# Performance work log

Hardware: AMD Instinct MI355X
Metric: run time of the kernel (lower is better)

## Reference

```python
import jax, jax.numpy as jnp
import numpy as np

N = 50000   # nodes
E = 1600000 # edges
D = 128     # input_dim
H = 128     # hidden_dim
O = 128     # output_dim
G = 64      # graphs in batch
EPS = 1e-5  # batchnorm eps


def setup_inputs() -> dict:
    key = jax.random.key(0)
    ks = jax.random.split(key, 20)
    x = jax.random.normal(ks[0], (N, D), jnp.float32)
    edge_index = jax.random.randint(ks[1], (2, E), 0, N, dtype=jnp.int32)
    batch = jnp.sort(jax.random.randint(ks[2], (N,), 0, G, dtype=jnp.int32))

    def lin(k, fi, fo):
        return jax.random.normal(k, (fi, fo), jnp.float32) / np.float32(np.sqrt(fi))

    return {
        "x": x, "edge_index": edge_index, "batch": batch,
        "W1": lin(ks[3], D, H), "b1": jnp.zeros((H,), jnp.float32),
        "W2": lin(ks[4], H, H), "b2": jnp.zeros((H,), jnp.float32),
        "W3": lin(ks[5], H, O), "b3": jnp.zeros((O,), jnp.float32),
        "g1": 1.0 + 0.1 * jax.random.normal(ks[6], (H,), jnp.float32),
        "be1": 0.1 * jax.random.normal(ks[7], (H,), jnp.float32),
        "rm1": 0.1 * jax.random.normal(ks[8], (H,), jnp.float32),
        "rv1": 0.5 + jax.random.uniform(ks[9], (H,), jnp.float32),
        "g2": 1.0 + 0.1 * jax.random.normal(ks[10], (H,), jnp.float32),
        "be2": 0.1 * jax.random.normal(ks[11], (H,), jnp.float32),
        "rm2": 0.1 * jax.random.normal(ks[12], (H,), jnp.float32),
        "rv2": 0.5 + jax.random.uniform(ks[13], (H,), jnp.float32),
    }


def _gcn_layer(h, W, b, row, col, norm):
    # h: [N, Fin] -> [N, Fout]; GCN: A_hat @ (h W) + b with sym-normalized A_hat
    h = h @ W
    msg = h[row] * norm[:, None]                      # [E+N, Fout] gather
    out = jax.ops.segment_sum(msg, col, num_segments=N)
    return out + b


def _bn_eval(h, g, be, rm, rv):
    return (h - rm) * jax.lax.rsqrt(rv + EPS) * g + be


def reference(x, edge_index, batch, W1, b1, W2, b2, W3, b3,
              g1, be1, rm1, rv1, g2, be2, rm2, rv2):
    # add self loops (PyG GCNConv default)
    loop = jnp.arange(N, dtype=edge_index.dtype)
    row = jnp.concatenate([edge_index[0], loop])
    col = jnp.concatenate([edge_index[1], loop])
    deg = jax.ops.segment_sum(jnp.ones_like(col, jnp.float32), col, num_segments=N)
    dinv = jnp.where(deg > 0, jax.lax.rsqrt(jnp.maximum(deg, 1.0)), 0.0)
    norm = dinv[row] * dinv[col]                       # [E+N]

    h = _gcn_layer(x, W1, b1, row, col, norm)
    h = jax.nn.relu(_bn_eval(h, g1, be1, rm1, rv1))    # dropout is identity (eval)
    h = _gcn_layer(h, W2, b2, row, col, norm)
    h = jax.nn.relu(_bn_eval(h, g2, be2, rm2, rv2))
    h = _gcn_layer(h, W3, b3, row, col, norm)
    # global_add_pool by graph id
    return jax.ops.segment_sum(h, batch, num_segments=G)  # [G, O]
```

## Files before the change

### kernel.cpp

```cpp
#include <hip/hip_runtime.h>
#include <hip/hip_bf16.h>

#define NN 50000
#define NROWS (NN + 1)
#define NE 1600000
#define NEPAD 1951024
#define DIM 128
#define NG 64
#define EPSV 1e-5f
#define NCHUNK 49
#define UNROLL 8
#define RUN 4
#define NXCD 8
#define SHARD_COLS (NN / NXCD)
#define FILL_CHUNKS 256

typedef __attribute__((ext_vector_type(8))) __bf16 bf16x8;
typedef __attribute__((ext_vector_type(2))) __bf16 bf16x2;
typedef __attribute__((ext_vector_type(16))) float f32x16;


__global__ void count_kernel(const int4* __restrict__ ecol4, int* __restrict__ cnt) {
    int i = blockIdx.x * 256 + threadIdx.x;
    if (i < NE / 4) {
        int4 c = ecol4[i];
        atomicAdd(&cnt[c.x], 1);
        atomicAdd(&cnt[c.y], 1);
        atomicAdd(&cnt[c.z], 1);
        atomicAdd(&cnt[c.w], 1);
    }
}

__global__ void scan_chunk(const int* __restrict__ cnt, int* __restrict__ excl,
                           int* __restrict__ csum) {
    __shared__ int lds[256];
    int t = threadIdx.x;
    int base = blockIdx.x * 1024 + t * 4;
    int v0 = (base + 0 < NN) ? ((cnt[base + 0] + 7) & ~7) : 0;
    int v1 = (base + 1 < NN) ? ((cnt[base + 1] + 7) & ~7) : 0;
    int v2 = (base + 2 < NN) ? ((cnt[base + 2] + 7) & ~7) : 0;
    int v3 = (base + 3 < NN) ? ((cnt[base + 3] + 7) & ~7) : 0;
    int s = v0 + v1 + v2 + v3;
    lds[t] = s;
    __syncthreads();
    for (int off = 1; off < 256; off <<= 1) {
        int x = (t >= off) ? lds[t - off] : 0;
        __syncthreads();
        lds[t] += x;
        __syncthreads();
    }
    int run = lds[t] - s;
    if (t == 255) csum[blockIdx.x] = lds[t];
    if (base + 0 < NN) excl[base + 0] = run; run += v0;
    if (base + 1 < NN) excl[base + 1] = run; run += v1;
    if (base + 2 < NN) excl[base + 2] = run; run += v2;
    if (base + 3 < NN) excl[base + 3] = run;
}

__global__ void scan_tail(const int* __restrict__ csum, int* __restrict__ coff,
                          int* __restrict__ row_ptr, int nch) {
    int l = threadIdx.x;
    int v = (l < nch) ? csum[l] : 0;
    int s = v;
    for (int o = 1; o < 64; o <<= 1) {
        int x = __shfl_up(s, o);
        if (l >= o) s += x;
    }
    if (l < nch) coff[l] = s - v;
    if (l == nch - 1) row_ptr[NN] = s;
}

__global__ void fixup_kernel(int* __restrict__ row_ptr, const int* __restrict__ coff,
                             const int* __restrict__ cnt, float* __restrict__ dinv,
                             int* __restrict__ cursor) {
    int n = blockIdx.x * 256 + threadIdx.x;
    if (n < NN) {
        int rp = row_ptr[n] + coff[n >> 10];
        row_ptr[n] = rp;
        cursor[n] = rp;
        dinv[n] = rsqrtf((float)(cnt[n] + 1));
    }
}

__global__ void sentinel_kernel(int4* __restrict__ esrc4) {
    const int4 v = {NN, NN, NN, NN};
    for (int i = blockIdx.x * 256 + threadIdx.x; i < NEPAD / 4; i += gridDim.x * 256)
        esrc4[i] = v;
}

__global__ void fill_kernel(const int* __restrict__ erow, const int* __restrict__ ecol,
                            int* __restrict__ cursor, int* __restrict__ esrc) {
    const int shard = blockIdx.x & (NXCD - 1);
    const int chunk = blockIdx.x >> 3;
    const int lo = shard * SHARD_COLS;
    const int hi = lo + SHARD_COLS;
    for (int e = chunk * 256 + threadIdx.x; e < NE; e += FILL_CHUNKS * 256) {
        const int c = ecol[e];
        if (c >= lo && c < hi) {
            int pos = atomicAdd(&cursor[c], 1);
            esrc[pos] = erow[e];
        }
    }
}

__global__ void bn_prep_kernel(const float* __restrict__ b1, const float* __restrict__ g1,
                               const float* __restrict__ be1, const float* __restrict__ rm1,
                               const float* __restrict__ rv1,
                               const float* __restrict__ b2, const float* __restrict__ g2,
                               const float* __restrict__ be2, const float* __restrict__ rm2,
                               const float* __restrict__ rv2,
                               float* __restrict__ sc1, float* __restrict__ sh1,
                               float* __restrict__ sc2, float* __restrict__ sh2,
                               __bf16* __restrict__ tbuf) {
    int c = threadIdx.x;
    if (c < DIM) {
        float s1 = g1[c] * rsqrtf(rv1[c] + EPSV);
        sc1[c] = s1;
        sh1[c] = (b1[c] - rm1[c]) * s1 + be1[c];
        float s2 = g2[c] * rsqrtf(rv2[c] + EPSV);
        sc2[c] = s2;
        sh2[c] = (b2[c] - rm2[c]) * s2 + be2[c];
        tbuf[(size_t)NN * DIM + c] = (__bf16)0.f;
    }
}


__device__ __forceinline__ bf16x8 load8(const float* p) {
    float4 lo = ((const float4*)p)[0], hi = ((const float4*)p)[1];
    bf16x8 a;
    a[0] = (__bf16)lo.x; a[1] = (__bf16)lo.y; a[2] = (__bf16)lo.z; a[3] = (__bf16)lo.w;
    a[4] = (__bf16)hi.x; a[5] = (__bf16)hi.y; a[6] = (__bf16)hi.z; a[7] = (__bf16)hi.w;
    return a;
}
__device__ __forceinline__ bf16x8 load8(const __bf16* p) {
    return *(const bf16x8*)p;
}

template <typename T>
__global__ void __launch_bounds__(256) matmul_kernel(const T* __restrict__ h,
                                                     const float* __restrict__ W,
                                                     const float* __restrict__ dinv,
                                                     __bf16* __restrict__ t) {
    const int wave = threadIdx.x >> 6;
    const int lane = threadIdx.x & 63;
    const int col = wave * 32 + (lane & 31);
    const int khalf = (lane >> 5) * 8;

    bf16x8 b[8];
#pragma unroll
    for (int kc = 0; kc < 8; kc++) {
#pragma unroll
        for (int j = 0; j < 8; j++) {
            b[kc][j] = (__bf16)W[(kc * 16 + khalf + j) * DIM + col];
        }
    }

    const int ntiles = (NN + 31) / 32;
    for (int tile = blockIdx.x; tile < ntiles; tile += gridDim.x) {
        const int arow = tile * 32 + (lane & 31);
        const int arow_c = (arow < NN) ? arow : (NN - 1);
        f32x16 acc = {};
#pragma unroll
        for (int kc = 0; kc < 8; kc++) {
            bf16x8 a = load8(h + (size_t)arow_c * DIM + kc * 16 + khalf);
            acc = __builtin_amdgcn_mfma_f32_32x32x16_bf16(a, b[kc], acc, 0, 0, 0);
        }
#pragma unroll
        for (int r = 0; r < 16; r++) {
            int orow = tile * 32 + (r & 3) + 8 * (r >> 2) + 4 * (lane >> 5);
            if (orow < NN) t[(size_t)orow * DIM + col] = (__bf16)(acc[r] * dinv[orow]);
        }
    }
}


__device__ __forceinline__ float lo16(unsigned u) { return __uint_as_float(u << 16); }
__device__ __forceinline__ float hi16(unsigned u) { return __uint_as_float(u & 0xffff0000u); }

__device__ __forceinline__ void gather_core(
    const unsigned* __restrict__ t32, const int* __restrict__ esrc,
    int beg, int end, int lane, float& ax, float& ay) {
    for (int e = beg; e < end; e += UNROLL) {
        int s[UNROLL];
        unsigned u[UNROLL];
#pragma unroll
        for (int i = 0; i < UNROLL; i++) s[i] = esrc[e + i];
#pragma unroll
        for (int i = 0; i < UNROLL; i++) {
            const unsigned idx = ((unsigned)s[i] << 6) + lane;
            u[i] = t32[idx];
        }
#pragma unroll
        for (int i = 0; i < UNROLL; i++) {
            ax += lo16(u[i]);
            ay += hi16(u[i]);
        }
    }
}

__global__ void __launch_bounds__(256) gather_bn_kernel(
    const unsigned* __restrict__ t32, const int* __restrict__ row_ptr,
    const int* __restrict__ esrc, const float* __restrict__ dinv,
    const float* __restrict__ scale, const float* __restrict__ shift,
    __bf16* __restrict__ out) {
    const int lane = threadIdx.x & 63;
    const int n = __builtin_amdgcn_readfirstlane(blockIdx.x * 4 + (threadIdx.x >> 6));
    if (n >= NN) return;
    float ax = 0.f, ay = 0.f;
    const int beg = row_ptr[n], end = row_ptr[n + 1];
    gather_core(t32, esrc, beg, end, lane, ax, ay);
    {
        const unsigned u = t32[((unsigned)n << 6) + lane];
        ax += lo16(u); ay += hi16(u);
    }
    const float dv = dinv[n];
    const int c0 = lane * 2, c1 = c0 + 1;
    const float vx = fmaxf(fmaf(ax, dv * scale[c0], shift[c0]), 0.f);
    const float vy = fmaxf(fmaf(ay, dv * scale[c1], shift[c1]), 0.f);
    bf16x2 o; o[0] = (__bf16)vx; o[1] = (__bf16)vy;
    *(bf16x2*)(out + (size_t)n * DIM + c0) = o;
}


__global__ void __launch_bounds__(256) gather_pool_kernel(
    const unsigned* __restrict__ t32, const int* __restrict__ row_ptr,
    const int* __restrict__ esrc, const float* __restrict__ dinv,
    const float* __restrict__ bias, const int* __restrict__ batch,
    float* __restrict__ out) {
    const int lane = threadIdx.x & 63;
    const int wid = __builtin_amdgcn_readfirstlane(blockIdx.x * 4 + (threadIdx.x >> 6));
    const int n0 = wid * RUN;
    if (n0 >= NN) return;
    const int c0 = lane * 2, c1 = c0 + 1;
    const float bx = bias[c0], by = bias[c1];
    float rx = 0.f, ry = 0.f;
    int g = batch[n0];
    for (int j = 0; j < RUN; j++) {
        const int n = n0 + j;
        float ax = 0.f, ay = 0.f;
        const int beg = row_ptr[n], end = row_ptr[n + 1];
        gather_core(t32, esrc, beg, end, lane, ax, ay);
        {
            const unsigned u = t32[((unsigned)n << 6) + lane];
            ax += lo16(u); ay += hi16(u);
        }
        const float dv = dinv[n];
        const int gn = batch[n];
        if (gn != g) {
            atomicAdd(out + (size_t)g * DIM + c0, rx);
            atomicAdd(out + (size_t)g * DIM + c1, ry);
            rx = 0.f; ry = 0.f; g = gn;
        }
        rx += fmaf(ax, dv, bx);
        ry += fmaf(ay, dv, by);
    }
    atomicAdd(out + (size_t)g * DIM + c0, rx);
    atomicAdd(out + (size_t)g * DIM + c1, ry);
}


extern "C" void kernel_launch(void* const* d_in, const int* in_sizes, int n_in,
                              void* d_out, int out_size, void* d_ws, size_t ws_size,
                              hipStream_t stream) {
    const float* x    = (const float*)d_in[0];
    const int*   ei   = (const int*)d_in[1];
    const int*   batch= (const int*)d_in[2];
    const float* W1 = (const float*)d_in[3];
    const float* b1 = (const float*)d_in[4];
    const float* W2 = (const float*)d_in[5];
    const float* b2 = (const float*)d_in[6];
    const float* W3 = (const float*)d_in[7];
    const float* b3 = (const float*)d_in[8];
    const float* g1 = (const float*)d_in[9];
    const float* be1= (const float*)d_in[10];
    const float* rm1= (const float*)d_in[11];
    const float* rv1= (const float*)d_in[12];
    const float* g2 = (const float*)d_in[13];
    const float* be2= (const float*)d_in[14];
    const float* rm2= (const float*)d_in[15];
    const float* rv2= (const float*)d_in[16];
    const int* erow = ei;
    const int* ecol = ei + NE;

    char* ws = (char*)d_ws;
    size_t off = 0;
    auto alloc = [&](size_t bytes) -> void* {
        void* p = ws + off;
        off = (off + bytes + 255) & ~(size_t)255;
        return p;
    };
    int*    cnt     = (int*)alloc(NN * sizeof(int));
    int*    row_ptr = (int*)alloc((NN + 1) * sizeof(int));
    int*    cursor  = (int*)alloc(NN * sizeof(int));
    int*    csum    = (int*)alloc(64 * sizeof(int));
    int*    coff    = (int*)alloc(64 * sizeof(int));
    float*  dinv    = (float*)alloc(NN * sizeof(float));
    int*    esrc    = (int*)alloc(NEPAD * sizeof(int));
    __bf16* tbuf    = (__bf16*)alloc((size_t)NROWS * DIM * sizeof(__bf16));
    __bf16* hbuf    = (__bf16*)alloc((size_t)NN * DIM * sizeof(__bf16));
    float*  sc1     = (float*)alloc(DIM * sizeof(float));
    float*  sh1     = (float*)alloc(DIM * sizeof(float));
    float*  sc2     = (float*)alloc(DIM * sizeof(float));
    float*  sh2     = (float*)alloc(DIM * sizeof(float));

    hipMemsetAsync(cnt, 0, NN * sizeof(int), stream);
    hipMemsetAsync(d_out, 0, NG * DIM * sizeof(float), stream);

    bn_prep_kernel<<<1, 128, 0, stream>>>(b1, g1, be1, rm1, rv1,
                                          b2, g2, be2, rm2, rv2,
                                          sc1, sh1, sc2, sh2, tbuf);
    sentinel_kernel<<<1024, 256, 0, stream>>>((int4*)esrc);
    count_kernel<<<(NE / 4 + 255) / 256, 256, 0, stream>>>((const int4*)ecol, cnt);
    scan_chunk<<<NCHUNK, 256, 0, stream>>>(cnt, row_ptr, csum);
    scan_tail<<<1, 64, 0, stream>>>(csum, coff, row_ptr, NCHUNK);
    fixup_kernel<<<(NN + 255) / 256, 256, 0, stream>>>(row_ptr, coff, cnt, dinv, cursor);
    fill_kernel<<<NXCD * FILL_CHUNKS, 256, 0, stream>>>(erow, ecol, cursor, esrc);

    const unsigned* t32 = (const unsigned*)tbuf;
    const int nblk = (NN + 3) / 4;
    const int nblk_pool = (NN / RUN + 3) / 4;

    matmul_kernel<float><<<512, 256, 0, stream>>>(x, W1, dinv, tbuf);
    gather_bn_kernel<<<nblk, 256, 0, stream>>>(t32, row_ptr, esrc, dinv,
                                               sc1, sh1, hbuf);
    matmul_kernel<__bf16><<<512, 256, 0, stream>>>(hbuf, W2, dinv, tbuf);
    gather_bn_kernel<<<nblk, 256, 0, stream>>>(t32, row_ptr, esrc, dinv,
                                               sc2, sh2, hbuf);
    matmul_kernel<__bf16><<<512, 256, 0, stream>>>(hbuf, W3, dinv, tbuf);
    gather_pool_kernel<<<nblk_pool, 256, 0, stream>>>(t32, row_ptr, esrc, dinv,
                                                      b3, batch, (float*)d_out);
}
```

Measured before the change: 385.5 us.

## Gather neighbor rows with 16-byte loads across four edge groups per wave

The gather kernels now split each wave into four 16-lane groups. Each lane loads a uint4 (8 bf16 features), so one wave fetches 4 neighbor rows per load instead of one row via 32-bit loads. Partial sums are reduced with xor shuffles, and only 16 lanes finish the BN/ReLU or pooling and write vectorized outputs. The aim is fewer, wider memory transactions per edge and more gather parallelism, at the cost of extra shuffles and idle lanes in the epilogue. Separately, the sentinel fill is fused into the count kernel to save a launch.

```diff
diff --git a/kernel.cpp b/kernel.cpp
--- a/kernel.cpp
+++ b/kernel.cpp
@@ -9,25 +9,34 @@
 #define NG 64
 #define EPSV 1e-5f
 #define NCHUNK 49
-#define UNROLL 8
 #define RUN 4
 #define NXCD 8
 #define SHARD_COLS (NN / NXCD)
 #define FILL_CHUNKS 256
+#define SENT_BLOCKS 512
 
 typedef __attribute__((ext_vector_type(8))) __bf16 bf16x8;
 typedef __attribute__((ext_vector_type(2))) __bf16 bf16x2;
 typedef __attribute__((ext_vector_type(16))) float f32x16;
 
 
-__global__ void count_kernel(const int4* __restrict__ ecol4, int* __restrict__ cnt) {
-    int i = blockIdx.x * 256 + threadIdx.x;
-    if (i < NE / 4) {
-        int4 c = ecol4[i];
-        atomicAdd(&cnt[c.x], 1);
-        atomicAdd(&cnt[c.y], 1);
-        atomicAdd(&cnt[c.z], 1);
-        atomicAdd(&cnt[c.w], 1);
+__global__ void count_sent_kernel(const int4* __restrict__ ecol4,
+                                  int* __restrict__ cnt,
+                                  int4* __restrict__ esrc4) {
+    if (blockIdx.x < SENT_BLOCKS) {
+        const int4 v = {NN, NN, NN, NN};
+        for (int i = blockIdx.x * 256 + threadIdx.x; i < NEPAD / 4;
+             i += SENT_BLOCKS * 256)
+            esrc4[i] = v;
+    } else {
+        int i = (blockIdx.x - SENT_BLOCKS) * 256 + threadIdx.x;
+        if (i < NE / 4) {
+            int4 c = ecol4[i];
+            atomicAdd(&cnt[c.x], 1);
+            atomicAdd(&cnt[c.y], 1);
+            atomicAdd(&cnt[c.z], 1);
+            atomicAdd(&cnt[c.w], 1);
+        }
     }
 }
 
@@ -80,12 +89,6 @@
         cursor[n] = rp;
         dinv[n] = rsqrtf((float)(cnt[n] + 1));
     }
-}
-
-__global__ void sentinel_kernel(int4* __restrict__ esrc4) {
-    const int4 v = {NN, NN, NN, NN};
-    for (int i = blockIdx.x * 256 + threadIdx.x; i < NEPAD / 4; i += gridDim.x * 256)
-        esrc4[i] = v;
 }
 
 __global__ void fill_kernel(const int* __restrict__ erow, const int* __restrict__ ecol,
@@ -177,85 +180,116 @@
 __device__ __forceinline__ float lo16(unsigned u) { return __uint_as_float(u << 16); }
 __device__ __forceinline__ float hi16(unsigned u) { return __uint_as_float(u & 0xffff0000u); }
 
-__device__ __forceinline__ void gather_core(
-    const unsigned* __restrict__ t32, const int* __restrict__ esrc,
-    int beg, int end, int lane, float& ax, float& ay) {
-    for (int e = beg; e < end; e += UNROLL) {
-        int s[UNROLL];
-        unsigned u[UNROLL];
-#pragma unroll
-        for (int i = 0; i < UNROLL; i++) s[i] = esrc[e + i];
-#pragma unroll
-        for (int i = 0; i < UNROLL; i++) {
-            const unsigned idx = ((unsigned)s[i] << 6) + lane;
-            u[i] = t32[idx];
-        }
-#pragma unroll
-        for (int i = 0; i < UNROLL; i++) {
-            ax += lo16(u[i]);
-            ay += hi16(u[i]);
-        }
+__device__ __forceinline__ void accum8(uint4 u, float (&a)[8]) {
+    a[0] += lo16(u.x); a[1] += hi16(u.x);
+    a[2] += lo16(u.y); a[3] += hi16(u.y);
+    a[4] += lo16(u.z); a[5] += hi16(u.z);
+    a[6] += lo16(u.w); a[7] += hi16(u.w);
+}
+
+__device__ __forceinline__ void gather_core4(
+    const uint4* __restrict__ tp4, const int* __restrict__ esrc,
+    int beg, int end, int grp, int sub, float (&a)[8]) {
+    for (int e = beg; e < end; e += 8) {
+        const int s0 = esrc[e + grp];
+        const int s1 = esrc[e + 4 + grp];
+        const uint4 u0 = tp4[(unsigned)s0 * 16u + sub];
+        const uint4 u1 = tp4[(unsigned)s1 * 16u + sub];
+        accum8(u0, a);
+        accum8(u1, a);
     }
 }
 
 __global__ void __launch_bounds__(256) gather_bn_kernel(
-    const unsigned* __restrict__ t32, const int* __restrict__ row_ptr,
+    const uint4* __restrict__ tp4, const int* __restrict__ row_ptr,
     const int* __restrict__ esrc, const float* __restrict__ dinv,
     const float* __restrict__ scale, const float* __restrict__ shift,
     __bf16* __restrict__ out) {
     const int lane = threadIdx.x & 63;
+    const int grp = lane >> 4, sub = lane & 15;
     const int n = __builtin_amdgcn_readfirstlane(blockIdx.x * 4 + (threadIdx.x >> 6));
     if (n >= NN) return;
-    float ax = 0.f, ay = 0.f;
+    float a[8] = {};
     const int beg = row_ptr[n], end = row_ptr[n + 1];
-    gather_core(t32, esrc, beg, end, lane, ax, ay);
-    {
-        const unsigned u = t32[((unsigned)n << 6) + lane];
-        ax += lo16(u); ay += hi16(u);
-    }
-    const float dv = dinv[n];
-    const int c0 = lane * 2, c1 = c0 + 1;
-    const float vx = fmaxf(fmaf(ax, dv * scale[c0], shift[c0]), 0.f);
-    const float vy = fmaxf(fmaf(ay, dv * scale[c1], shift[c1]), 0.f);
-    bf16x2 o; o[0] = (__bf16)vx; o[1] = (__bf16)vy;
-    *(bf16x2*)(out + (size_t)n * DIM + c0) = o;
+    gather_core4(tp4, esrc, beg, end, grp, sub, a);
+#pragma unroll
+    for (int i = 0; i < 8; i++) {
+        a[i] += __shfl_xor(a[i], 16);
+        a[i] += __shfl_xor(a[i], 32);
+    }
+    if (lane < 16) {
+        accum8(tp4[(unsigned)n * 16u + sub], a);
+        const float dv = dinv[n];
+        const int c0 = sub * 8;
+        float4 s0 = *(const float4*)(scale + c0), s1 = *(const float4*)(scale + c0 + 4);
+        float4 h0 = *(const float4*)(shift + c0), h1 = *(const float4*)(shift + c0 + 4);
+        bf16x8 o;
+        o[0] = (__bf16)fmaxf(fmaf(a[0], dv * s0.x, h0.x), 0.f);
+        o[1] = (__bf16)fmaxf(fmaf(a[1], dv * s0.y, h0.y), 0.f);
+        o[2] = (__bf16)fmaxf(fmaf(a[2], dv * s0.z, h0.z), 0.f);
+        o[3] = (__bf16)fmaxf(fmaf(a[3], dv * s0.w, h0.w), 0.f);
+        o[4] = (__bf16)fmaxf(fmaf(a[4], dv * s1.x, h1.x), 0.f);
+        o[5] = (__bf16)fmaxf(fmaf(a[5], dv * s1.y, h1.y), 0.f);
+        o[6] = (__bf16)fmaxf(fmaf(a[6], dv * s1.z, h1.z), 0.f);
+        o[7] = (__bf16)fmaxf(fmaf(a[7], dv * s1.w, h1.w), 0.f);
+        *(bf16x8*)(out + (size_t)n * DIM + c0) = o;
+    }
 }
 
 
 __global__ void __launch_bounds__(256) gather_pool_kernel(
-    const unsigned* __restrict__ t32, const int* __restrict__ row_ptr,
+    const uint4* __restrict__ tp4, const int* __restrict__ row_ptr,
     const int* __restrict__ esrc, const float* __restrict__ dinv,
     const float* __restrict__ bias, const int* __restrict__ batch,
     float* __restrict__ out) {
     const int lane = threadIdx.x & 63;
+    const int grp = lane >> 4, sub = lane & 15;
     const int wid = __builtin_amdgcn_readfirstlane(blockIdx.x * 4 + (threadIdx.x >> 6));
     const int n0 = wid * RUN;
     if (n0 >= NN) return;
-    const int c0 = lane * 2, c1 = c0 + 1;
-    const float bx = bias[c0], by = bias[c1];
-    float rx = 0.f, ry = 0.f;
+    const int c0 = sub * 8;
+    float4 b0 = *(const float4*)(bias + c0), b1v = *(const float4*)(bias + c0 + 4);
+    float rx[8] = {};
     int g = batch[n0];
     for (int j = 0; j < RUN; j++) {
         const int n = n0 + j;
-        float ax = 0.f, ay = 0.f;
+        float a[8] = {};
         const int beg = row_ptr[n], end = row_ptr[n + 1];
-        gather_core(t32, esrc, beg, end, lane, ax, ay);
-        {
-            const unsigned u = t32[((unsigned)n << 6) + lane];
-            ax += lo16(u); ay += hi16(u);
+        gather_core4(tp4, esrc, beg, end, grp, sub, a);
+#pragma unroll
+        for (int i = 0; i < 8; i++) {
+            a[i] += __shfl_xor(a[i], 16);
+            a[i] += __shfl_xor(a[i], 32);
         }
         const float dv = dinv[n];
         const int gn = batch[n];
         if (gn != g) {
-            atomicAdd(out + (size_t)g * DIM + c0, rx);
-            atomicAdd(out + (size_t)g * DIM + c1, ry);
-            rx = 0.f; ry = 0.f; g = gn;
-        }
-        rx += fmaf(ax, dv, bx);
-        ry += fmaf(ay, dv, by);
-    }
-    atomicAdd(out + (size_t)g * DIM + c0, rx);
-    atomicAdd(out + (size_t)g * DIM + c1, ry);
+            if (lane < 16) {
+                float* op = out + (size_t)g * DIM + c0;
+#pragma unroll
+                for (int i = 0; i < 8; i++) atomicAdd(op + i, rx[i]);
+            }
+#pragma unroll
+            for (int i = 0; i < 8; i++) rx[i] = 0.f;
+            g = gn;
+        }
+        if (lane < 16) {
+            accum8(tp4[(unsigned)n * 16u + sub], a);
+            rx[0] += fmaf(a[0], dv, b0.x);
+            rx[1] += fmaf(a[1], dv, b0.y);
+            rx[2] += fmaf(a[2], dv, b0.z);
+            rx[3] += fmaf(a[3], dv, b0.w);
+            rx[4] += fmaf(a[4], dv, b1v.x);
+            rx[5] += fmaf(a[5], dv, b1v.y);
+            rx[6] += fmaf(a[6], dv, b1v.z);
+            rx[7] += fmaf(a[7], dv, b1v.w);
+        }
+    }
+    if (lane < 16) {
+        float* op = out + (size_t)g * DIM + c0;
+#pragma unroll
+        for (int i = 0; i < 8; i++) atomicAdd(op + i, rx[i]);
+    }
 }
 
 
@@ -309,24 +343,24 @@
     bn_prep_kernel<<<1, 128, 0, stream>>>(b1, g1, be1, rm1, rv1,
                                           b2, g2, be2, rm2, rv2,
                                           sc1, sh1, sc2, sh2, tbuf);
-    sentinel_kernel<<<1024, 256, 0, stream>>>((int4*)esrc);
-    count_kernel<<<(NE / 4 + 255) / 256, 256, 0, stream>>>((const int4*)ecol, cnt);
+    count_sent_kernel<<<SENT_BLOCKS + (NE / 4 + 255) / 256, 256, 0, stream>>>(
+        (const int4*)ecol, cnt, (int4*)esrc);
     scan_chunk<<<NCHUNK, 256, 0, stream>>>(cnt, row_ptr, csum);
     scan_tail<<<1, 64, 0, stream>>>(csum, coff, row_ptr, NCHUNK);
     fixup_kernel<<<(NN + 255) / 256, 256, 0, stream>>>(row_ptr, coff, cnt, dinv, cursor);
     fill_kernel<<<NXCD * FILL_CHUNKS, 256, 0, stream>>>(erow, ecol, cursor, esrc);
 
-    const unsigned* t32 = (const unsigned*)tbuf;
+    const uint4* tp4 = (const uint4*)tbuf;
     const int nblk = (NN + 3) / 4;
     const int nblk_pool = (NN / RUN + 3) / 4;
 
     matmul_kernel<float><<<512, 256, 0, stream>>>(x, W1, dinv, tbuf);
-    gather_bn_kernel<<<nblk, 256, 0, stream>>>(t32, row_ptr, esrc, dinv,
+    gather_bn_kernel<<<nblk, 256, 0, stream>>>(tp4, row_ptr, esrc, dinv,
                                                sc1, sh1, hbuf);
     matmul_kernel<__bf16><<<512, 256, 0, stream>>>(hbuf, W2, dinv, tbuf);
-    gather_bn_kernel<<<nblk, 256, 0, stream>>>(t32, row_ptr, esrc, dinv,
+    gather_bn_kernel<<<nblk, 256, 0, stream>>>(tp4, row_ptr, esrc, dinv,
                                                sc2, sh2, hbuf);
     matmul_kernel<__bf16><<<512, 256, 0, stream>>>(hbuf, W3, dinv, tbuf);
-    gather_pool_kernel<<<nblk_pool, 256, 0, stream>>>(t32, row_ptr, esrc, dinv,
+    gather_pool_kernel<<<nblk_pool, 256, 0, stream>>>(tp4, row_ptr, esrc, dinv,
                                                       b3, batch, (float*)d_out);
 }
```

New measurement: 474.3 us. 23.0% more time.

## Bucket edges by column shard during counting so fill reads only its shard

Applied to the files above, without the earlier changes.

The separate count pass is merged into a staging kernel that counts in-degrees and also buckets each (col,row) pair into a per-shard staging array, using block-local LDS counters and a global per-shard tail. The fill kernel then reads only its own shard's staged pairs instead of scanning all edges eight times and discarding most of them. This trades an extra 8-byte-per-edge write and read of staging plus several block barriers per chunk for far less redundant edge reading during fill. The sentinel grid is also halved.

```diff
diff --git a/kernel.cpp b/kernel.cpp
--- a/kernel.cpp
+++ b/kernel.cpp
@@ -13,21 +13,46 @@
 #define RUN 4
 #define NXCD 8
 #define SHARD_COLS (NN / NXCD)
-#define FILL_CHUNKS 256
+#define SHARD_CAP 220000
+#define STG_BLOCKS 1024
+#define FILL2_CHUNKS 128
 
 typedef __attribute__((ext_vector_type(8))) __bf16 bf16x8;
 typedef __attribute__((ext_vector_type(2))) __bf16 bf16x2;
 typedef __attribute__((ext_vector_type(16))) float f32x16;
 
 
-__global__ void count_kernel(const int4* __restrict__ ecol4, int* __restrict__ cnt) {
-    int i = blockIdx.x * 256 + threadIdx.x;
-    if (i < NE / 4) {
-        int4 c = ecol4[i];
-        atomicAdd(&cnt[c.x], 1);
-        atomicAdd(&cnt[c.y], 1);
-        atomicAdd(&cnt[c.z], 1);
-        atomicAdd(&cnt[c.w], 1);
+__global__ void sentinel_kernel(int4* __restrict__ esrc4) {
+    const int4 v = {NN, NN, NN, NN};
+    for (int i = blockIdx.x * 256 + threadIdx.x; i < NEPAD / 4; i += gridDim.x * 256)
+        esrc4[i] = v;
+}
+
+__global__ void __launch_bounds__(256) stage_kernel(
+    const int* __restrict__ erow, const int* __restrict__ ecol,
+    int* __restrict__ cnt, int* __restrict__ shard_tail,
+    int2* __restrict__ staging) {
+    __shared__ int lcnt[NXCD];
+    __shared__ int lbase[NXCD];
+    __shared__ int lpos[NXCD];
+    const int t = threadIdx.x;
+    const int nchunks = NE / 256;
+    for (int chunk = blockIdx.x; chunk < nchunks; chunk += gridDim.x) {
+        const int e = chunk * 256 + t;
+        const int c = ecol[e];
+        const int r = erow[e];
+        atomicAdd(&cnt[c], 1);
+        const int sh = c / SHARD_COLS;
+        if (t < NXCD) { lcnt[t] = 0; lpos[t] = 0; }
+        __syncthreads();
+        atomicAdd(&lcnt[sh], 1);
+        __syncthreads();
+        if (t < NXCD) lbase[t] = atomicAdd(&shard_tail[t], lcnt[t]);
+        __syncthreads();
+        const int p = lbase[sh] + atomicAdd(&lpos[sh], 1);
+        int2 pr; pr.x = c; pr.y = r;
+        staging[(size_t)sh * SHARD_CAP + p] = pr;
+        __syncthreads();
     }
 }
 
@@ -82,24 +107,17 @@
     }
 }
 
-__global__ void sentinel_kernel(int4* __restrict__ esrc4) {
-    const int4 v = {NN, NN, NN, NN};
-    for (int i = blockIdx.x * 256 + threadIdx.x; i < NEPAD / 4; i += gridDim.x * 256)
-        esrc4[i] = v;
-}
-
-__global__ void fill_kernel(const int* __restrict__ erow, const int* __restrict__ ecol,
-                            int* __restrict__ cursor, int* __restrict__ esrc) {
-    const int shard = blockIdx.x & (NXCD - 1);
+__global__ void __launch_bounds__(256) fill2_kernel(
+    const int2* __restrict__ staging, const int* __restrict__ shard_tail,
+    int* __restrict__ cursor, int* __restrict__ esrc) {
+    const int sh = blockIdx.x & (NXCD - 1);
     const int chunk = blockIdx.x >> 3;
-    const int lo = shard * SHARD_COLS;
-    const int hi = lo + SHARD_COLS;
-    for (int e = chunk * 256 + threadIdx.x; e < NE; e += FILL_CHUNKS * 256) {
-        const int c = ecol[e];
-        if (c >= lo && c < hi) {
-            int pos = atomicAdd(&cursor[c], 1);
-            esrc[pos] = erow[e];
-        }
+    const int m = shard_tail[sh];
+    const int2* __restrict__ sp = staging + (size_t)sh * SHARD_CAP;
+    for (int i = chunk * 256 + threadIdx.x; i < m; i += FILL2_CHUNKS * 256) {
+        const int2 pr = sp[i];
+        const int pos = atomicAdd(&cursor[pr.x], 1);
+        esrc[pos] = pr.y;
     }
 }
 
@@ -295,7 +313,9 @@
     int*    csum    = (int*)alloc(64 * sizeof(int));
     int*    coff    = (int*)alloc(64 * sizeof(int));
     float*  dinv    = (float*)alloc(NN * sizeof(float));
+    int*    stail   = (int*)alloc(NXCD * sizeof(int));
     int*    esrc    = (int*)alloc(NEPAD * sizeof(int));
+    int2*   staging = (int2*)alloc((size_t)NXCD * SHARD_CAP * sizeof(int2));
     __bf16* tbuf    = (__bf16*)alloc((size_t)NROWS * DIM * sizeof(__bf16));
     __bf16* hbuf    = (__bf16*)alloc((size_t)NN * DIM * sizeof(__bf16));
     float*  sc1     = (float*)alloc(DIM * sizeof(float));
@@ -304,17 +324,18 @@
     float*  sh2     = (float*)alloc(DIM * sizeof(float));
 
     hipMemsetAsync(cnt, 0, NN * sizeof(int), stream);
+    hipMemsetAsync(stail, 0, NXCD * sizeof(int), stream);
     hipMemsetAsync(d_out, 0, NG * DIM * sizeof(float), stream);
 
     bn_prep_kernel<<<1, 128, 0, stream>>>(b1, g1, be1, rm1, rv1,
                                           b2, g2, be2, rm2, rv2,
                                           sc1, sh1, sc2, sh2, tbuf);
-    sentinel_kernel<<<1024, 256, 0, stream>>>((int4*)esrc);
-    count_kernel<<<(NE / 4 + 255) / 256, 256, 0, stream>>>((const int4*)ecol, cnt);
+    sentinel_kernel<<<512, 256, 0, stream>>>((int4*)esrc);
+    stage_kernel<<<STG_BLOCKS, 256, 0, stream>>>(erow, ecol, cnt, stail, staging);
     scan_chunk<<<NCHUNK, 256, 0, stream>>>(cnt, row_ptr, csum);
     scan_tail<<<1, 64, 0, stream>>>(csum, coff, row_ptr, NCHUNK);
     fixup_kernel<<<(NN + 255) / 256, 256, 0, stream>>>(row_ptr, coff, cnt, dinv, cursor);
-    fill_kernel<<<NXCD * FILL_CHUNKS, 256, 0, stream>>>(erow, ecol, cursor, esrc);
+    fill2_kernel<<<NXCD * FILL2_CHUNKS, 256, 0, stream>>>(staging, stail, cursor, esrc);
 
     const unsigned* t32 = (const unsigned*)tbuf;
     const int nblk = (NN + 3) / 4;
```

New measurement: 409.6 us. 6.3% more time.
